# Performance work log

Measured on AMD Instinct MI355X. Metric: run time of the kernel, lower is better.

Reference implementation:

```python
import jax, jax.numpy as jnp
import numpy as np

DIM_Q = 1024
DIM_K = 1024
DIM_V = 1024


def setup_inputs() -> dict:
    key = jax.random.key(0)
    kx, kq, kk, kv = jax.random.split(key, 4)
    x = jax.random.normal(kx, (4, 2048, DIM_Q), dtype=jnp.float32)
    # torch nn.Linear weights: [out_features, in_features], y = x @ W.T
    scale = 1.0 / np.sqrt(DIM_Q)
    Wq = jax.random.uniform(kq, (DIM_K, DIM_Q), dtype=jnp.float32, minval=-scale, maxval=scale)
    Wk = jax.random.uniform(kk, (DIM_K, DIM_Q), dtype=jnp.float32, minval=-scale, maxval=scale)
    Wv = jax.random.uniform(kv, (DIM_V, DIM_Q), dtype=jnp.float32, minval=-scale, maxval=scale)
    return {"x": x, "Wq": Wq, "Wk": Wk, "Wv": Wv}


def reference(x, Wq, Wk, Wv):
    # q, k: [b, s, dim_k]; v: [b, s, dim_v]
    q = jnp.einsum('bsd,kd->bsk', x, Wq)
    k = jnp.einsum('bsd,kd->bsk', x, Wk)
    v = jnp.einsum('bsd,vd->bsv', x, Wv)
    norm_fact = 1.0 / jnp.sqrt(jnp.asarray(DIM_K, dtype=x.dtype))
    score = jnp.einsum('bik,bjk->bij', q, k) * norm_fact  # [b, s, s]
    score = jax.nn.softmax(score, axis=-1)
    att = jnp.einsum('bij,bjv->biv', score, v)
    att = att + v  # is_residual=True
    return att
```

## Files before the change

### kernel.cpp

```cpp
#include <hip/hip_runtime.h>
#include <hip/hip_bf16.h>

using bf16 = __hip_bfloat16;
typedef __attribute__((ext_vector_type(8))) short short8;
typedef __attribute__((ext_vector_type(4))) float floatx4;
typedef __attribute__((ext_vector_type(8))) int int8v;

__device__ __forceinline__ void async_ld16(const void* g, void* l) {
  __builtin_amdgcn_global_load_lds((const __attribute__((address_space(1))) void*)g,
                                   (__attribute__((address_space(3))) void*)l, 16, 0, 0);
}

__device__ __forceinline__ int pk4_fp8(float a, float b, float c, float d) {
  int v = __builtin_amdgcn_cvt_pk_fp8_f32(a, b, 0, false);
  return __builtin_amdgcn_cvt_pk_fp8_f32(c, d, v, true);
}

__device__ __forceinline__ int8v ld_frag16(const unsigned char* lo, const unsigned char* hi) {
  int4 l0 = *(const int4*)lo, h0 = *(const int4*)hi;
  int8v v;
  v[0] = l0.x; v[1] = l0.y; v[2] = l0.z; v[3] = l0.w;
  v[4] = h0.x; v[5] = h0.y; v[6] = h0.z; v[7] = h0.w;
  return v;
}


__device__ __forceinline__ void gemm_core(const bf16* __restrict__ At,
                                          const bf16* __restrict__ Bt,
                                          int K, bf16* lA, bf16* lB,
                                          floatx4 acc[4][4]) {
  const int tid  = threadIdx.x;
  const int w    = tid >> 6;
  const int lane = tid & 63;
  const int subM = (w >> 1) * 64;
  const int subN = (w & 1) * 64;
  const int fr   = lane & 15;
  const int fq   = lane >> 4;

  int srow[4], scol[4], sdst[4];
#pragma unroll
  for (int q = 0; q < 4; ++q) {
    int p = q * 256 + w * 64 + lane;
    int r = p >> 3;
    int j = (p & 7) ^ (r & 7);
    srow[q] = r;
    scol[q] = j * 8;
    sdst[q] = (q * 256 + w * 64) * 8;
  }
  int offA[2][4], offB[2][4];
#pragma unroll
  for (int kc = 0; kc < 2; ++kc)
#pragma unroll
    for (int i = 0; i < 4; ++i) {
      int rA = subM + i * 16 + fr;
      offA[kc][i] = (rA * 8 + ((kc * 4 + fq) ^ (rA & 7))) * 8;
      int rB = subN + i * 16 + fr;
      offB[kc][i] = (rB * 8 + ((kc * 4 + fq) ^ (rB & 7))) * 8;
    }

  floatx4 zero = {0.f, 0.f, 0.f, 0.f};
#pragma unroll
  for (int i = 0; i < 4; ++i)
#pragma unroll
    for (int j = 0; j < 4; ++j) acc[i][j] = zero;

  for (int k0 = 0; k0 < K; k0 += 64) {
    __syncthreads();
#pragma unroll
    for (int q = 0; q < 4; ++q) {
      async_ld16(At + (size_t)srow[q] * K + k0 + scol[q], lA + sdst[q]);
      async_ld16(Bt + (size_t)srow[q] * K + k0 + scol[q], lB + sdst[q]);
    }
    __syncthreads();
#pragma unroll
    for (int kc = 0; kc < 2; ++kc) {
      short8 a[4], b[4];
#pragma unroll
      for (int i = 0; i < 4; ++i) a[i] = *(const short8*)(lA + offA[kc][i]);
#pragma unroll
      for (int j = 0; j < 4; ++j) b[j] = *(const short8*)(lB + offB[kc][j]);
#pragma unroll
      for (int i = 0; i < 4; ++i)
#pragma unroll
        for (int j = 0; j < 4; ++j)
          acc[i][j] = __builtin_amdgcn_mfma_f32_16x16x32_bf16(a[i], b[j], acc[i][j], 0, 0, 0);
    }
  }
}

__device__ __forceinline__ void gemm_core_f8(const unsigned char* __restrict__ At,
                                             const unsigned char* __restrict__ Bt,
                                             int K, unsigned char* lA, unsigned char* lB,
                                             floatx4 acc[4][4]) {
  const int tid  = threadIdx.x;
  const int w    = tid >> 6;
  const int lane = tid & 63;
  const int subM = (w >> 1) * 64;
  const int subN = (w & 1) * 64;
  const int fr   = lane & 15;
  const int fq   = lane >> 4;

  int srow[4], scol[4], sdst[4];
#pragma unroll
  for (int q = 0; q < 4; ++q) {
    int p = q * 256 + w * 64 + lane;
    int r = p >> 3;
    int j = (p & 7) ^ (r & 7) ^ ((r & 8) >> 1);
    srow[q] = r;
    scol[q] = j * 16;
    sdst[q] = (q * 256 + w * 64) * 16;
  }
  int offA[2][4], offB[2][4];
#pragma unroll
  for (int h = 0; h < 2; ++h)
#pragma unroll
    for (int i = 0; i < 4; ++i) {
      int rA = subM + i * 16 + fr;
      offA[h][i] = rA * 128 + (((fq * 2 + h) ^ (rA & 7) ^ ((rA & 8) >> 1)) * 16);
      int rB = subN + i * 16 + fr;
      offB[h][i] = rB * 128 + (((fq * 2 + h) ^ (rB & 7) ^ ((rB & 8) >> 1)) * 16);
    }

  floatx4 zero = {0.f, 0.f, 0.f, 0.f};
#pragma unroll
  for (int i = 0; i < 4; ++i)
#pragma unroll
    for (int j = 0; j < 4; ++j) acc[i][j] = zero;

  for (int k0 = 0; k0 < K; k0 += 128) {
    __syncthreads();
#pragma unroll
    for (int q = 0; q < 4; ++q) {
      async_ld16(At + (size_t)srow[q] * K + k0 + scol[q], lA + sdst[q]);
      async_ld16(Bt + (size_t)srow[q] * K + k0 + scol[q], lB + sdst[q]);
    }
    __syncthreads();
    int8v a[4], b[4];
#pragma unroll
    for (int i = 0; i < 4; ++i) a[i] = ld_frag16(lA + offA[0][i], lA + offA[1][i]);
#pragma unroll
    for (int j = 0; j < 4; ++j) b[j] = ld_frag16(lB + offB[0][j], lB + offB[1][j]);
#pragma unroll
    for (int i = 0; i < 4; ++i)
#pragma unroll
      for (int j = 0; j < 4; ++j)
        acc[i][j] = __builtin_amdgcn_mfma_scale_f32_16x16x128_f8f6f4(
            a[i], b[j], acc[i][j], 0, 0, 0, 0x7F7F7F7F, 0, 0x7F7F7F7F);
  }
}

__device__ __forceinline__ void gemm_core_f8_v2(const unsigned char* __restrict__ At,
                                                const unsigned char* __restrict__ Bt,
                                                int K, unsigned char* lA, unsigned char* lB,
                                                floatx4 acc[4][8]) {
  const int tid  = threadIdx.x;
  const int w    = tid >> 6;
  const int lane = tid & 63;
  const int subM = (w >> 1) * 64;
  const int subN = (w & 1) * 128;
  const int fr   = lane & 15;
  const int fq   = lane >> 4;

  int srowA[4], scolA[4], sdstA[4];
#pragma unroll
  for (int q = 0; q < 4; ++q) {
    int p = q * 256 + w * 64 + lane;
    int r = p >> 3;
    int j = (p & 7) ^ (r & 7) ^ ((r & 8) >> 1);
    srowA[q] = r; scolA[q] = j * 16; sdstA[q] = (q * 256 + w * 64) * 16;
  }
  int srowB[8], scolB[8], sdstB[8];
#pragma unroll
  for (int q = 0; q < 8; ++q) {
    int p = q * 256 + w * 64 + lane;
    int r = p >> 3;
    int j = (p & 7) ^ (r & 7) ^ ((r & 8) >> 1);
    srowB[q] = r; scolB[q] = j * 16; sdstB[q] = (q * 256 + w * 64) * 16;
  }
  int offA[2][4], offB[2][8];
#pragma unroll
  for (int h = 0; h < 2; ++h) {
#pragma unroll
    for (int i = 0; i < 4; ++i) {
      int rA = subM + i * 16 + fr;
      offA[h][i] = rA * 128 + (((fq * 2 + h) ^ (rA & 7) ^ ((rA & 8) >> 1)) * 16);
    }
#pragma unroll
    for (int j = 0; j < 8; ++j) {
      int rB = subN + j * 16 + fr;
      offB[h][j] = rB * 128 + (((fq * 2 + h) ^ (rB & 7) ^ ((rB & 8) >> 1)) * 16);
    }
  }

  floatx4 zero = {0.f, 0.f, 0.f, 0.f};
#pragma unroll
  for (int i = 0; i < 4; ++i)
#pragma unroll
    for (int j = 0; j < 8; ++j) acc[i][j] = zero;

  for (int k0 = 0; k0 < K; k0 += 128) {
    __syncthreads();
#pragma unroll
    for (int q = 0; q < 4; ++q)
      async_ld16(At + (size_t)srowA[q] * K + k0 + scolA[q], lA + sdstA[q]);
#pragma unroll
    for (int q = 0; q < 8; ++q)
      async_ld16(Bt + (size_t)srowB[q] * K + k0 + scolB[q], lB + sdstB[q]);
    __syncthreads();
    int8v a[4];
#pragma unroll
    for (int i = 0; i < 4; ++i) a[i] = ld_frag16(lA + offA[0][i], lA + offA[1][i]);
#pragma unroll
    for (int j = 0; j < 8; ++j) {
      int8v bf = ld_frag16(lB + offB[0][j], lB + offB[1][j]);
#pragma unroll
      for (int i = 0; i < 4; ++i)
        acc[i][j] = __builtin_amdgcn_mfma_scale_f32_16x16x128_f8f6f4(
            a[i], bf, acc[i][j], 0, 0, 0, 0x7F7F7F7F, 0, 0x7F7F7F7F);
    }
  }
}

__global__ __launch_bounds__(256, 2) void proj_gemm(
    const bf16* __restrict__ Xbf, const bf16* __restrict__ Wvbf, bf16* __restrict__ Vbf,
    const unsigned char* __restrict__ X8, const unsigned char* __restrict__ Wq8,
    const unsigned char* __restrict__ Wk8,
    unsigned char* __restrict__ Qf8, unsigned char* __restrict__ Kf8,
    unsigned char* __restrict__ Vt8) {
  __shared__ __align__(16) char lds[49152];
  const int id = blockIdx.x;
  const int tid = threadIdx.x, w = tid >> 6, lane = tid & 63;
  const int fr = lane & 15, fq = lane >> 4;

  if (id < 512) {
    const int r = id & 7, g = id >> 3;
    const int ty = r * 8 + (g & 7), tx = g >> 3;
    bf16* lA = (bf16*)lds;
    bf16* lB = (bf16*)(lds + 16384);
    floatx4 acc[4][4];
    gemm_core(Xbf + (size_t)ty * 128 * 1024, Wvbf + (size_t)tx * 128 * 1024,
              1024, lA, lB, acc);
    const int subM = (w >> 1) * 64, subN = (w & 1) * 64;
    const int rowBase = ty * 128 + subM;
    const int colBase = tx * 128 + subN;
#pragma unroll
    for (int i = 0; i < 4; ++i)
#pragma unroll
      for (int j = 0; j < 4; ++j)
#pragma unroll
        for (int rr = 0; rr < 4; ++rr) {
          int row = rowBase + i * 16 + fq * 4 + rr;
          int col = colBase + j * 16 + fr;
          Vbf[(size_t)row * 1024 + col] = __float2bfloat16(acc[i][j][rr]);
        }

    __syncthreads();
    unsigned int* tp = (unsigned int*)lds;
#pragma unroll
    for (int i = 0; i < 4; ++i) {
      int rw = (subM + i * 16 + fq * 4) >> 2;
#pragma unroll
      for (int j = 0; j < 4; ++j) {
        int c = subN + j * 16 + fr;
        tp[c * 32 + (rw ^ (c & 31))] =
            (unsigned int)pk4_fp8(acc[i][j][0], acc[i][j][1], acc[i][j][2], acc[i][j][3]);
      }
    }
    __syncthreads();
    const int vrow = tid >> 1;
    const int gh = tid & 1;
    size_t ob = ((size_t)((ty >> 4) * 1024 + tx * 128 + vrow)) * 2048 +
                (size_t)(ty & 15) * 128 + gh * 64;
#pragma unroll
    for (int h = 0; h < 4; ++h) {
      unsigned int W0 = tp[vrow * 32 + ((gh * 16 + h) ^ (vrow & 31))];
      unsigned int W1 = tp[vrow * 32 + ((gh * 16 + h + 4) ^ (vrow & 31))];
      unsigned int W2 = tp[vrow * 32 + ((gh * 16 + h + 8) ^ (vrow & 31))];
      unsigned int W3 = tp[vrow * 32 + ((gh * 16 + h + 12) ^ (vrow & 31))];
      unsigned int t01l = __builtin_amdgcn_perm(W1, W0, 0x05010400u);
      unsigned int t01h = __builtin_amdgcn_perm(W1, W0, 0x07030602u);
      unsigned int t23l = __builtin_amdgcn_perm(W3, W2, 0x05010400u);
      unsigned int t23h = __builtin_amdgcn_perm(W3, W2, 0x07030602u);
      uint4 o;
      o.x = __builtin_amdgcn_perm(t23l, t01l, 0x05040100u);
      o.y = __builtin_amdgcn_perm(t23l, t01l, 0x07060302u);
      o.z = __builtin_amdgcn_perm(t23h, t01h, 0x05040100u);
      o.w = __builtin_amdgcn_perm(t23h, t01h, 0x07060302u);
      *(uint4*)&Vt8[ob + h * 16] = o;
    }
  } else {
    const int local = id - 512;
    const int z = local >> 8, lid = local & 255;
    const int r = lid & 7, g = lid >> 3;
    const int ty = r * 8 + (g & 7);
    const int tx = g >> 3;
    unsigned char* lA = (unsigned char*)lds;
    unsigned char* lB = (unsigned char*)(lds + 16384);
    floatx4 acc[4][8];
    gemm_core_f8_v2(X8 + (size_t)ty * 128 * 1024,
                    (z == 0 ? Wq8 : Wk8) + (size_t)tx * 256 * 1024, 1024, lA, lB, acc);
    unsigned char* dst = (z == 0) ? Qf8 : Kf8;
    const int subM = (w >> 1) * 64, subN = (w & 1) * 128;
    const int rowBase = ty * 128 + subM;
    const int colBase = tx * 256 + subN;
#pragma unroll
    for (int i = 0; i < 4; ++i)
#pragma unroll
      for (int rr = 0; rr < 4; ++rr) {
        int row = rowBase + i * 16 + fq * 4 + rr;
        unsigned int p0 = (unsigned int)pk4_fp8(acc[i][0][rr], acc[i][1][rr],
                                                acc[i][2][rr], acc[i][3][rr]);
        unsigned int p1 = (unsigned int)pk4_fp8(acc[i][4][rr], acc[i][5][rr],
                                                acc[i][6][rr], acc[i][7][rr]);
        *(unsigned int*)&dst[(size_t)row * 1024 + colBase + fr * 4] = p0;
        *(unsigned int*)&dst[(size_t)row * 1024 + colBase + 64 + fr * 4] = p1;
      }
  }
}

__global__ __launch_bounds__(256, 2) void mid_kernel(
    const unsigned char* __restrict__ Qf8, const unsigned char* __restrict__ Kf8,
    unsigned char* __restrict__ S8, float* __restrict__ l) {
  __shared__ __align__(16) char lds[49152];
  const int id = blockIdx.x;
  const int t = threadIdx.x;

  const int r = id & 7, g = id >> 3;
  const int b = g >> 4;
  const int rem = g & 15;
  const int ty = r * 2 + (rem & 1);
  const int tx = rem >> 1;
  unsigned char* lA = (unsigned char*)lds;
  unsigned char* lB = (unsigned char*)(lds + 16384);
  floatx4 acc[4][8];
  gemm_core_f8_v2(Qf8 + (size_t)b * 2048 * 1024 + (size_t)ty * 128 * 1024,
                  Kf8 + (size_t)b * 2048 * 1024 + (size_t)tx * 256 * 1024,
                  1024, lA, lB, acc);
  const int w = t >> 6, lane = t & 63;
  const int subM = (w >> 1) * 64, subN = (w & 1) * 128;
  const int fr = lane & 15, fq = lane >> 4;
  const int rowBase = ty * 128 + subM;
  const int colBase = tx * 256 + subN;
  unsigned char* Sb = S8 + (size_t)b * 2048 * 2048;
  float* lb = l + (size_t)b * 2048;
#pragma unroll
  for (int i = 0; i < 4; ++i)
#pragma unroll
    for (int rr = 0; rr < 4; ++rr) {
      int row = rowBase + i * 16 + fq * 4 + rr;
      unsigned int p0 = (unsigned int)pk4_fp8(
          __expf(acc[i][0][rr] * 0.03125f), __expf(acc[i][1][rr] * 0.03125f),
          __expf(acc[i][2][rr] * 0.03125f), __expf(acc[i][3][rr] * 0.03125f));
      unsigned int p1 = (unsigned int)pk4_fp8(
          __expf(acc[i][4][rr] * 0.03125f), __expf(acc[i][5][rr] * 0.03125f),
          __expf(acc[i][6][rr] * 0.03125f), __expf(acc[i][7][rr] * 0.03125f));
      *(unsigned int*)&Sb[(size_t)row * 2048 + colBase + fr * 4] = p0;
      *(unsigned int*)&Sb[(size_t)row * 2048 + colBase + 64 + fr * 4] = p1;
      float psum = __builtin_amdgcn_cvt_f32_fp8(p0, 0) + __builtin_amdgcn_cvt_f32_fp8(p0, 1) +
                   __builtin_amdgcn_cvt_f32_fp8(p0, 2) + __builtin_amdgcn_cvt_f32_fp8(p0, 3) +
                   __builtin_amdgcn_cvt_f32_fp8(p1, 0) + __builtin_amdgcn_cvt_f32_fp8(p1, 1) +
                   __builtin_amdgcn_cvt_f32_fp8(p1, 2) + __builtin_amdgcn_cvt_f32_fp8(p1, 3);
      psum += __shfl_xor(psum, 1, 64);
      psum += __shfl_xor(psum, 2, 64);
      psum += __shfl_xor(psum, 4, 64);
      psum += __shfl_xor(psum, 8, 64);
      if (fr == 0) atomicAdd(&lb[row], psum);
    }
}

__global__ __launch_bounds__(256, 2) void pv_gemm(const unsigned char* __restrict__ S8,
                                                  const unsigned char* __restrict__ Vt8,
                                                  const bf16* __restrict__ Vbf,
                                                  const float* __restrict__ l,
                                                  float* __restrict__ out) {
  __shared__ __align__(16) char lds[32768];
  unsigned char* lA = (unsigned char*)lds;
  unsigned char* lB = (unsigned char*)(lds + 16384);
  const int id = blockIdx.x;
  const int r = id & 7, g = id >> 3;
  const int b = g >> 4;
  const int rem = g & 15;
  const int ty = r * 2 + (rem & 1);
  const int tx = rem >> 1;

  floatx4 acc[4][4];
  gemm_core_f8(S8 + (size_t)b * 2048 * 2048 + (size_t)ty * 128 * 2048,
               Vt8 + (size_t)b * 1024 * 2048 + (size_t)tx * 128 * 2048,
               2048, lA, lB, acc);

  const int tid = threadIdx.x, w = tid >> 6, lane = tid & 63;
  const int subM = (w >> 1) * 64, subN = (w & 1) * 64;
  const int fr = lane & 15, fq = lane >> 4;
  const int rowBase = ty * 128 + subM;
  const int colBase = tx * 128 + subN;
  const float* lb = l + (size_t)b * 2048;
#pragma unroll
  for (int i = 0; i < 4; ++i)
#pragma unroll
    for (int rr = 0; rr < 4; ++rr) {
      int row = rowBase + i * 16 + fq * 4 + rr;
      float inv = 1.0f / lb[row];
#pragma unroll
      for (int j = 0; j < 4; ++j) {
        int col = colBase + j * 16 + fr;
        size_t oi = ((size_t)b * 2048 + row) * 1024 + col;
        out[oi] = acc[i][j][rr] * inv + __bfloat162float(Vbf[oi]);
      }
    }
}

__global__ void cast_all(const float* __restrict__ x, const float* __restrict__ wq,
                         const float* __restrict__ wk, const float* __restrict__ wv,
                         bf16* __restrict__ Xbf, unsigned char* __restrict__ X8,
                         unsigned char* __restrict__ Wq8, unsigned char* __restrict__ Wk8,
                         bf16* __restrict__ Wvbf, float* __restrict__ l) {
  const int blk = blockIdx.x;
  const int t = threadIdx.x;
  if (blk < 2048) {
#pragma unroll
    for (int k = 0; k < 4; ++k) {
      int i = blk * 1024 + k * 256 + t;
      float4 f = ((const float4*)x)[i];
      bf16 tmp[4] = {__float2bfloat16(f.x), __float2bfloat16(f.y),
                     __float2bfloat16(f.z), __float2bfloat16(f.w)};
      ((ushort4*)Xbf)[i] = *(const ushort4*)tmp;
      ((unsigned int*)X8)[i] = (unsigned int)pk4_fp8(f.x, f.y, f.z, f.w);
    }
  } else if (blk < 2560) {
    const float* src = (blk < 2304) ? wq : wk;
    unsigned char* dst = (blk < 2304) ? Wq8 : Wk8;
    int base = ((blk - 2048) & 255) * 1024;
#pragma unroll
    for (int k = 0; k < 4; ++k) {
      int i = base + k * 256 + t;
      float4 f = ((const float4*)src)[i];
      ((unsigned int*)dst)[i] = (unsigned int)pk4_fp8(f.x, f.y, f.z, f.w);
    }
  } else if (blk < 2816) {
#pragma unroll
    for (int k = 0; k < 4; ++k) {
      int i = (blk - 2560) * 1024 + k * 256 + t;
      float4 f = ((const float4*)wv)[i];
      bf16 tmp[4] = {__float2bfloat16(f.x), __float2bfloat16(f.y),
                     __float2bfloat16(f.z), __float2bfloat16(f.w)};
      ((ushort4*)Wvbf)[i] = *(const ushort4*)tmp;
    }
  } else {
#pragma unroll
    for (int k = 0; k < 8; ++k)
      ((float4*)l)[k * 256 + t] = make_float4(0.f, 0.f, 0.f, 0.f);
  }
}

extern "C" void kernel_launch(void* const* d_in, const int* in_sizes, int n_in,
                              void* d_out, int out_size, void* d_ws, size_t ws_size,
                              hipStream_t stream) {
  const float* x  = (const float*)d_in[0];
  const float* Wq = (const float*)d_in[1];
  const float* Wk = (const float*)d_in[2];
  const float* Wv = (const float*)d_in[3];
  float* out = (float*)d_out;

  char* ws = (char*)d_ws;
  bf16* Xbf = (bf16*)ws;                   ws += (size_t)8192 * 1024 * 2;
  unsigned char* X8 = (unsigned char*)ws;  ws += (size_t)8192 * 1024;
  unsigned char* Wq8 = (unsigned char*)ws; ws += (size_t)1024 * 1024;
  unsigned char* Wk8 = (unsigned char*)ws; ws += (size_t)1024 * 1024;
  bf16* Wvbf = (bf16*)ws;                  ws += (size_t)1024 * 1024 * 2;
  unsigned char* Qf8 = (unsigned char*)ws; ws += (size_t)8192 * 1024;
  unsigned char* Kf8 = (unsigned char*)ws; ws += (size_t)8192 * 1024;
  bf16* Vbf = (bf16*)ws;                   ws += (size_t)8192 * 1024 * 2;
  unsigned char* Vt8 = (unsigned char*)ws; ws += (size_t)4 * 1024 * 2048;
  unsigned char* S8  = (unsigned char*)ws; ws += (size_t)4 * 2048 * 2048;
  float* l = (float*)ws;                   ws += (size_t)8192 * 4;

  cast_all<<<2817, 256, 0, stream>>>(x, Wq, Wk, Wv, Xbf, X8, Wq8, Wk8, Wvbf, l);
  proj_gemm<<<1024, 256, 0, stream>>>(Xbf, Wvbf, Vbf, X8, Wq8, Wk8, Qf8, Kf8, Vt8);
  mid_kernel<<<512, 256, 0, stream>>>(Qf8, Kf8, S8, l);
  pv_gemm<<<512, 256, 0, stream>>>(S8, Vt8, Vbf, l, out);
}
```

Before: 179.7 us.

## Use 256x256 double-buffered 8-wave FP8 GEMM core with phased prefetch for QK and scores

Replaces the single-buffered 128x256 FP8 GEMM core with a 256x256, 512-thread variant. It double-buffers LDS (128KB) and splits each K-step into four MFMA phases interleaved with fragment loads and async prefetch of the next tile, using barriers and setprio. The V projection is split out of the fused projection kernel into its own launch, and the Q/K projection and score kernels move to 256 larger blocks. This aims to hide global-load latency and raise data reuse per block, at the cost of one extra launch, lower occupancy from the large LDS, and fewer blocks to fill the CUs.

```diff
diff --git a/kernel.cpp b/kernel.cpp
--- a/kernel.cpp
+++ b/kernel.cpp
@@ -149,217 +149,268 @@
   }
 }
 
-__device__ __forceinline__ void gemm_core_f8_v2(const unsigned char* __restrict__ At,
-                                                const unsigned char* __restrict__ Bt,
-                                                int K, unsigned char* lA, unsigned char* lB,
-                                                floatx4 acc[4][8]) {
+__device__ __forceinline__ void gemm_core_f8_8ph(const unsigned char* __restrict__ At,
+                                                 const unsigned char* __restrict__ Bt,
+                                                 int K, unsigned char* lds0,
+                                                 floatx4 acc[8][4]) {
   const int tid  = threadIdx.x;
   const int w    = tid >> 6;
   const int lane = tid & 63;
-  const int subM = (w >> 1) * 64;
-  const int subN = (w & 1) * 128;
+  const int wr   = w >> 2;
+  const int wc   = w & 3;
+  const int subM = wr * 128;
+  const int subN = wc * 64;
   const int fr   = lane & 15;
   const int fq   = lane >> 4;
 
-  int srowA[4], scolA[4], sdstA[4];
+  int srcOff[4], dstOff[4];
 #pragma unroll
   for (int q = 0; q < 4; ++q) {
-    int p = q * 256 + w * 64 + lane;
+    int p = q * 512 + tid;
     int r = p >> 3;
     int j = (p & 7) ^ (r & 7) ^ ((r & 8) >> 1);
-    srowA[q] = r; scolA[q] = j * 16; sdstA[q] = (q * 256 + w * 64) * 16;
-  }
-  int srowB[8], scolB[8], sdstB[8];
-#pragma unroll
-  for (int q = 0; q < 8; ++q) {
-    int p = q * 256 + w * 64 + lane;
-    int r = p >> 3;
-    int j = (p & 7) ^ (r & 7) ^ ((r & 8) >> 1);
-    srowB[q] = r; scolB[q] = j * 16; sdstB[q] = (q * 256 + w * 64) * 16;
-  }
-  int offA[2][4], offB[2][8];
+    srcOff[q] = r * K + j * 16;
+    dstOff[q] = p * 16;
+  }
+  int offA[2][8], offB[2][4];
 #pragma unroll
   for (int h = 0; h < 2; ++h) {
 #pragma unroll
-    for (int i = 0; i < 4; ++i) {
+    for (int i = 0; i < 8; ++i) {
       int rA = subM + i * 16 + fr;
       offA[h][i] = rA * 128 + (((fq * 2 + h) ^ (rA & 7) ^ ((rA & 8) >> 1)) * 16);
     }
 #pragma unroll
-    for (int j = 0; j < 8; ++j) {
+    for (int j = 0; j < 4; ++j) {
       int rB = subN + j * 16 + fr;
       offB[h][j] = rB * 128 + (((fq * 2 + h) ^ (rB & 7) ^ ((rB & 8) >> 1)) * 16);
     }
   }
 
+  auto stageA = [&](int buf, int k0) {
+#pragma unroll
+    for (int q = 0; q < 4; ++q)
+      async_ld16(At + (size_t)(k0 + srcOff[q]), lds0 + buf * 65536 + dstOff[q]);
+  };
+  auto stageB = [&](int buf, int k0) {
+#pragma unroll
+    for (int q = 0; q < 4; ++q)
+      async_ld16(Bt + (size_t)(k0 + srcOff[q]), lds0 + buf * 65536 + 32768 + dstOff[q]);
+  };
+
   floatx4 zero = {0.f, 0.f, 0.f, 0.f};
 #pragma unroll
-  for (int i = 0; i < 4; ++i)
-#pragma unroll
-    for (int j = 0; j < 8; ++j) acc[i][j] = zero;
-
-  for (int k0 = 0; k0 < K; k0 += 128) {
-    __syncthreads();
-#pragma unroll
-    for (int q = 0; q < 4; ++q)
-      async_ld16(At + (size_t)srowA[q] * K + k0 + scolA[q], lA + sdstA[q]);
-#pragma unroll
-    for (int q = 0; q < 8; ++q)
-      async_ld16(Bt + (size_t)srowB[q] * K + k0 + scolB[q], lB + sdstB[q]);
-    __syncthreads();
-    int8v a[4];
+  for (int i = 0; i < 8; ++i)
+#pragma unroll
+    for (int j = 0; j < 4; ++j) acc[i][j] = zero;
+
+  stageA(0, 0);
+  stageB(0, 0);
+  asm volatile("s_waitcnt vmcnt(0)" ::: "memory");
+  __builtin_amdgcn_s_barrier();
+
+  const int nt = K >> 7;
+  for (int t = 0; t < nt; ++t) {
+    const unsigned char* lA = lds0 + (t & 1) * 65536;
+    const unsigned char* lB = lA + 32768;
+    const int nb = (t + 1) & 1;
+    const int k0n = (t + 1) << 7;
+    const bool pf = (t + 1) < nt;
+    int8v a[4], b0[2], b1[2];
+
 #pragma unroll
     for (int i = 0; i < 4; ++i) a[i] = ld_frag16(lA + offA[0][i], lA + offA[1][i]);
 #pragma unroll
-    for (int j = 0; j < 8; ++j) {
-      int8v bf = ld_frag16(lB + offB[0][j], lB + offB[1][j]);
-#pragma unroll
-      for (int i = 0; i < 4; ++i)
+    for (int j = 0; j < 2; ++j) b0[j] = ld_frag16(lB + offB[0][j], lB + offB[1][j]);
+    if (pf) stageA(nb, k0n);
+    __builtin_amdgcn_s_barrier();
+    asm volatile("s_waitcnt lgkmcnt(0)" ::: "memory");
+    __builtin_amdgcn_sched_barrier(0);
+    __builtin_amdgcn_s_setprio(1);
+#pragma unroll
+    for (int i = 0; i < 4; ++i)
+#pragma unroll
+      for (int j = 0; j < 2; ++j)
         acc[i][j] = __builtin_amdgcn_mfma_scale_f32_16x16x128_f8f6f4(
-            a[i], bf, acc[i][j], 0, 0, 0, 0x7F7F7F7F, 0, 0x7F7F7F7F);
-    }
-  }
-}
-
-__global__ __launch_bounds__(256, 2) void proj_gemm(
+            a[i], b0[j], acc[i][j], 0, 0, 0, 0x7F7F7F7F, 0, 0x7F7F7F7F);
+    __builtin_amdgcn_s_setprio(0);
+    __builtin_amdgcn_s_barrier();
+
+#pragma unroll
+    for (int j = 0; j < 2; ++j) b1[j] = ld_frag16(lB + offB[0][2 + j], lB + offB[1][2 + j]);
+    if (pf) stageB(nb, k0n);
+    __builtin_amdgcn_s_barrier();
+    asm volatile("s_waitcnt lgkmcnt(0)" ::: "memory");
+    __builtin_amdgcn_sched_barrier(0);
+    __builtin_amdgcn_s_setprio(1);
+#pragma unroll
+    for (int i = 0; i < 4; ++i)
+#pragma unroll
+      for (int j = 0; j < 2; ++j)
+        acc[i][2 + j] = __builtin_amdgcn_mfma_scale_f32_16x16x128_f8f6f4(
+            a[i], b1[j], acc[i][2 + j], 0, 0, 0, 0x7F7F7F7F, 0, 0x7F7F7F7F);
+    __builtin_amdgcn_s_setprio(0);
+    __builtin_amdgcn_s_barrier();
+
+#pragma unroll
+    for (int i = 0; i < 4; ++i) a[i] = ld_frag16(lA + offA[0][4 + i], lA + offA[1][4 + i]);
+    __builtin_amdgcn_s_barrier();
+    asm volatile("s_waitcnt lgkmcnt(0)" ::: "memory");
+    __builtin_amdgcn_sched_barrier(0);
+    __builtin_amdgcn_s_setprio(1);
+#pragma unroll
+    for (int i = 0; i < 4; ++i)
+#pragma unroll
+      for (int j = 0; j < 2; ++j)
+        acc[4 + i][2 + j] = __builtin_amdgcn_mfma_scale_f32_16x16x128_f8f6f4(
+            a[i], b1[j], acc[4 + i][2 + j], 0, 0, 0, 0x7F7F7F7F, 0, 0x7F7F7F7F);
+    __builtin_amdgcn_s_setprio(0);
+    __builtin_amdgcn_s_barrier();
+
+#pragma unroll
+    for (int j = 0; j < 2; ++j) b0[j] = ld_frag16(lB + offB[0][j], lB + offB[1][j]);
+    __builtin_amdgcn_s_barrier();
+    asm volatile("s_waitcnt lgkmcnt(0)" ::: "memory");
+    __builtin_amdgcn_sched_barrier(0);
+    __builtin_amdgcn_s_setprio(1);
+#pragma unroll
+    for (int i = 0; i < 4; ++i)
+#pragma unroll
+      for (int j = 0; j < 2; ++j)
+        acc[4 + i][j] = __builtin_amdgcn_mfma_scale_f32_16x16x128_f8f6f4(
+            a[i], b0[j], acc[4 + i][j], 0, 0, 0, 0x7F7F7F7F, 0, 0x7F7F7F7F);
+    __builtin_amdgcn_s_setprio(0);
+    asm volatile("s_waitcnt vmcnt(0)" ::: "memory");
+    __builtin_amdgcn_s_barrier();
+  }
+}
+
+__global__ __launch_bounds__(256, 2) void proj_v(
     const bf16* __restrict__ Xbf, const bf16* __restrict__ Wvbf, bf16* __restrict__ Vbf,
-    const unsigned char* __restrict__ X8, const unsigned char* __restrict__ Wq8,
-    const unsigned char* __restrict__ Wk8,
-    unsigned char* __restrict__ Qf8, unsigned char* __restrict__ Kf8,
     unsigned char* __restrict__ Vt8) {
   __shared__ __align__(16) char lds[49152];
   const int id = blockIdx.x;
   const int tid = threadIdx.x, w = tid >> 6, lane = tid & 63;
   const int fr = lane & 15, fq = lane >> 4;
 
-  if (id < 512) {
-    const int r = id & 7, g = id >> 3;
-    const int ty = r * 8 + (g & 7), tx = g >> 3;
-    bf16* lA = (bf16*)lds;
-    bf16* lB = (bf16*)(lds + 16384);
-    floatx4 acc[4][4];
-    gemm_core(Xbf + (size_t)ty * 128 * 1024, Wvbf + (size_t)tx * 128 * 1024,
-              1024, lA, lB, acc);
-    const int subM = (w >> 1) * 64, subN = (w & 1) * 64;
-    const int rowBase = ty * 128 + subM;
-    const int colBase = tx * 128 + subN;
-#pragma unroll
-    for (int i = 0; i < 4; ++i)
-#pragma unroll
-      for (int j = 0; j < 4; ++j)
-#pragma unroll
-        for (int rr = 0; rr < 4; ++rr) {
-          int row = rowBase + i * 16 + fq * 4 + rr;
-          int col = colBase + j * 16 + fr;
-          Vbf[(size_t)row * 1024 + col] = __float2bfloat16(acc[i][j][rr]);
-        }
-
-    __syncthreads();
-    unsigned int* tp = (unsigned int*)lds;
-#pragma unroll
-    for (int i = 0; i < 4; ++i) {
-      int rw = (subM + i * 16 + fq * 4) >> 2;
-#pragma unroll
-      for (int j = 0; j < 4; ++j) {
-        int c = subN + j * 16 + fr;
-        tp[c * 32 + (rw ^ (c & 31))] =
-            (unsigned int)pk4_fp8(acc[i][j][0], acc[i][j][1], acc[i][j][2], acc[i][j][3]);
-      }
-    }
-    __syncthreads();
-    const int vrow = tid >> 1;
-    const int gh = tid & 1;
-    size_t ob = ((size_t)((ty >> 4) * 1024 + tx * 128 + vrow)) * 2048 +
-                (size_t)(ty & 15) * 128 + gh * 64;
-#pragma unroll
-    for (int h = 0; h < 4; ++h) {
-      unsigned int W0 = tp[vrow * 32 + ((gh * 16 + h) ^ (vrow & 31))];
-      unsigned int W1 = tp[vrow * 32 + ((gh * 16 + h + 4) ^ (vrow & 31))];
-      unsigned int W2 = tp[vrow * 32 + ((gh * 16 + h + 8) ^ (vrow & 31))];
-      unsigned int W3 = tp[vrow * 32 + ((gh * 16 + h + 12) ^ (vrow & 31))];
-      unsigned int t01l = __builtin_amdgcn_perm(W1, W0, 0x05010400u);
-      unsigned int t01h = __builtin_amdgcn_perm(W1, W0, 0x07030602u);
-      unsigned int t23l = __builtin_amdgcn_perm(W3, W2, 0x05010400u);
-      unsigned int t23h = __builtin_amdgcn_perm(W3, W2, 0x07030602u);
-      uint4 o;
-      o.x = __builtin_amdgcn_perm(t23l, t01l, 0x05040100u);
-      o.y = __builtin_amdgcn_perm(t23l, t01l, 0x07060302u);
-      o.z = __builtin_amdgcn_perm(t23h, t01h, 0x05040100u);
-      o.w = __builtin_amdgcn_perm(t23h, t01h, 0x07060302u);
-      *(uint4*)&Vt8[ob + h * 16] = o;
-    }
-  } else {
-    const int local = id - 512;
-    const int z = local >> 8, lid = local & 255;
-    const int r = lid & 7, g = lid >> 3;
-    const int ty = r * 8 + (g & 7);
-    const int tx = g >> 3;
-    unsigned char* lA = (unsigned char*)lds;
-    unsigned char* lB = (unsigned char*)(lds + 16384);
-    floatx4 acc[4][8];
-    gemm_core_f8_v2(X8 + (size_t)ty * 128 * 1024,
-                    (z == 0 ? Wq8 : Wk8) + (size_t)tx * 256 * 1024, 1024, lA, lB, acc);
-    unsigned char* dst = (z == 0) ? Qf8 : Kf8;
-    const int subM = (w >> 1) * 64, subN = (w & 1) * 128;
-    const int rowBase = ty * 128 + subM;
-    const int colBase = tx * 256 + subN;
-#pragma unroll
-    for (int i = 0; i < 4; ++i)
+  const int r = id & 7, g = id >> 3;
+  const int ty = r * 8 + (g & 7), tx = g >> 3;
+  bf16* lA = (bf16*)lds;
+  bf16* lB = (bf16*)(lds + 16384);
+  floatx4 acc[4][4];
+  gemm_core(Xbf + (size_t)ty * 128 * 1024, Wvbf + (size_t)tx * 128 * 1024,
+            1024, lA, lB, acc);
+  const int subM = (w >> 1) * 64, subN = (w & 1) * 64;
+  const int rowBase = ty * 128 + subM;
+  const int colBase = tx * 128 + subN;
+#pragma unroll
+  for (int i = 0; i < 4; ++i)
+#pragma unroll
+    for (int j = 0; j < 4; ++j)
 #pragma unroll
       for (int rr = 0; rr < 4; ++rr) {
         int row = rowBase + i * 16 + fq * 4 + rr;
-        unsigned int p0 = (unsigned int)pk4_fp8(acc[i][0][rr], acc[i][1][rr],
-                                                acc[i][2][rr], acc[i][3][rr]);
-        unsigned int p1 = (unsigned int)pk4_fp8(acc[i][4][rr], acc[i][5][rr],
-                                                acc[i][6][rr], acc[i][7][rr]);
-        *(unsigned int*)&dst[(size_t)row * 1024 + colBase + fr * 4] = p0;
-        *(unsigned int*)&dst[(size_t)row * 1024 + colBase + 64 + fr * 4] = p1;
+        int col = colBase + j * 16 + fr;
+        Vbf[(size_t)row * 1024 + col] = __float2bfloat16(acc[i][j][rr]);
       }
-  }
-}
-
-__global__ __launch_bounds__(256, 2) void mid_kernel(
+
+  __syncthreads();
+  unsigned int* tp = (unsigned int*)lds;
+#pragma unroll
+  for (int i = 0; i < 4; ++i) {
+    int rw = (subM + i * 16 + fq * 4) >> 2;
+#pragma unroll
+    for (int j = 0; j < 4; ++j) {
+      int c = subN + j * 16 + fr;
+      tp[c * 32 + (rw ^ (c & 31))] =
+          (unsigned int)pk4_fp8(acc[i][j][0], acc[i][j][1], acc[i][j][2], acc[i][j][3]);
+    }
+  }
+  __syncthreads();
+  const int vrow = tid >> 1;
+  const int gh = tid & 1;
+  size_t ob = ((size_t)((ty >> 4) * 1024 + tx * 128 + vrow)) * 2048 +
+              (size_t)(ty & 15) * 128 + gh * 64;
+#pragma unroll
+  for (int h = 0; h < 4; ++h) {
+    unsigned int W0 = tp[vrow * 32 + ((gh * 16 + h) ^ (vrow & 31))];
+    unsigned int W1 = tp[vrow * 32 + ((gh * 16 + h + 4) ^ (vrow & 31))];
+    unsigned int W2 = tp[vrow * 32 + ((gh * 16 + h + 8) ^ (vrow & 31))];
+    unsigned int W3 = tp[vrow * 32 + ((gh * 16 + h + 12) ^ (vrow & 31))];
+    unsigned int t01l = __builtin_amdgcn_perm(W1, W0, 0x05010400u);
+    unsigned int t01h = __builtin_amdgcn_perm(W1, W0, 0x07030602u);
+    unsigned int t23l = __builtin_amdgcn_perm(W3, W2, 0x05010400u);
+    unsigned int t23h = __builtin_amdgcn_perm(W3, W2, 0x07030602u);
+    uint4 o;
+    o.x = __builtin_amdgcn_perm(t23l, t01l, 0x05040100u);
+    o.y = __builtin_amdgcn_perm(t23l, t01l, 0x07060302u);
+    o.z = __builtin_amdgcn_perm(t23h, t01h, 0x05040100u);
+    o.w = __builtin_amdgcn_perm(t23h, t01h, 0x07060302u);
+    *(uint4*)&Vt8[ob + h * 16] = o;
+  }
+}
+
+__global__ __launch_bounds__(512, 2) void proj_qk(
+    const unsigned char* __restrict__ X8, const unsigned char* __restrict__ Wq8,
+    const unsigned char* __restrict__ Wk8,
+    unsigned char* __restrict__ Qf8, unsigned char* __restrict__ Kf8) {
+  __shared__ __align__(16) char lds[131072];
+  const int id = blockIdx.x;
+  const int z = id >> 7, lid = id & 127;
+  const int ty = lid >> 2, tx = lid & 3;
+
+  floatx4 acc[8][4];
+  gemm_core_f8_8ph(X8 + (size_t)ty * 256 * 1024,
+                   (z == 0 ? Wq8 : Wk8) + (size_t)tx * 256 * 1024,
+                   1024, (unsigned char*)lds, acc);
+
+  unsigned char* dst = (z == 0) ? Qf8 : Kf8;
+  const int tid = threadIdx.x, w = tid >> 6, lane = tid & 63;
+  const int wr = w >> 2, wc = w & 3;
+  const int fr = lane & 15, fq = lane >> 4;
+  const int rowBase = ty * 256 + wr * 128;
+  const int colBase = tx * 256 + wc * 64;
+#pragma unroll
+  for (int i = 0; i < 8; ++i)
+#pragma unroll
+    for (int rr = 0; rr < 4; ++rr) {
+      int row = rowBase + i * 16 + fq * 4 + rr;
+      unsigned int p0 = (unsigned int)pk4_fp8(acc[i][0][rr], acc[i][1][rr],
+                                              acc[i][2][rr], acc[i][3][rr]);
+      *(unsigned int*)&dst[(size_t)row * 1024 + colBase + fr * 4] = p0;
+    }
+}
+
+__global__ __launch_bounds__(512, 2) void mid_kernel(
     const unsigned char* __restrict__ Qf8, const unsigned char* __restrict__ Kf8,
     unsigned char* __restrict__ S8, float* __restrict__ l) {
-  __shared__ __align__(16) char lds[49152];
+  __shared__ __align__(16) char lds[131072];
   const int id = blockIdx.x;
-  const int t = threadIdx.x;
-
-  const int r = id & 7, g = id >> 3;
-  const int b = g >> 4;
-  const int rem = g & 15;
-  const int ty = r * 2 + (rem & 1);
-  const int tx = rem >> 1;
-  unsigned char* lA = (unsigned char*)lds;
-  unsigned char* lB = (unsigned char*)(lds + 16384);
-  floatx4 acc[4][8];
-  gemm_core_f8_v2(Qf8 + (size_t)b * 2048 * 1024 + (size_t)ty * 128 * 1024,
-                  Kf8 + (size_t)b * 2048 * 1024 + (size_t)tx * 256 * 1024,
-                  1024, lA, lB, acc);
-  const int w = t >> 6, lane = t & 63;
-  const int subM = (w >> 1) * 64, subN = (w & 1) * 128;
+  const int b = id >> 6, ty = (id >> 3) & 7, tx = id & 7;
+
+  floatx4 acc[8][4];
+  gemm_core_f8_8ph(Qf8 + (size_t)b * 2048 * 1024 + (size_t)ty * 256 * 1024,
+                   Kf8 + (size_t)b * 2048 * 1024 + (size_t)tx * 256 * 1024,
+                   1024, (unsigned char*)lds, acc);
+
+  const int tid = threadIdx.x, w = tid >> 6, lane = tid & 63;
+  const int wr = w >> 2, wc = w & 3;
   const int fr = lane & 15, fq = lane >> 4;
-  const int rowBase = ty * 128 + subM;
-  const int colBase = tx * 256 + subN;
+  const int rowBase = ty * 256 + wr * 128;
+  const int colBase = tx * 256 + wc * 64;
   unsigned char* Sb = S8 + (size_t)b * 2048 * 2048;
   float* lb = l + (size_t)b * 2048;
 #pragma unroll
-  for (int i = 0; i < 4; ++i)
+  for (int i = 0; i < 8; ++i)
 #pragma unroll
     for (int rr = 0; rr < 4; ++rr) {
       int row = rowBase + i * 16 + fq * 4 + rr;
       unsigned int p0 = (unsigned int)pk4_fp8(
           __expf(acc[i][0][rr] * 0.03125f), __expf(acc[i][1][rr] * 0.03125f),
           __expf(acc[i][2][rr] * 0.03125f), __expf(acc[i][3][rr] * 0.03125f));
-      unsigned int p1 = (unsigned int)pk4_fp8(
-          __expf(acc[i][4][rr] * 0.03125f), __expf(acc[i][5][rr] * 0.03125f),
-          __expf(acc[i][6][rr] * 0.03125f), __expf(acc[i][7][rr] * 0.03125f));
       *(unsigned int*)&Sb[(size_t)row * 2048 + colBase + fr * 4] = p0;
-      *(unsigned int*)&Sb[(size_t)row * 2048 + colBase + 64 + fr * 4] = p1;
       float psum = __builtin_amdgcn_cvt_f32_fp8(p0, 0) + __builtin_amdgcn_cvt_f32_fp8(p0, 1) +
-                   __builtin_amdgcn_cvt_f32_fp8(p0, 2) + __builtin_amdgcn_cvt_f32_fp8(p0, 3) +
-                   __builtin_amdgcn_cvt_f32_fp8(p1, 0) + __builtin_amdgcn_cvt_f32_fp8(p1, 1) +
-                   __builtin_amdgcn_cvt_f32_fp8(p1, 2) + __builtin_amdgcn_cvt_f32_fp8(p1, 3);
+                   __builtin_amdgcn_cvt_f32_fp8(p0, 2) + __builtin_amdgcn_cvt_f32_fp8(p0, 3);
       psum += __shfl_xor(psum, 1, 64);
       psum += __shfl_xor(psum, 2, 64);
       psum += __shfl_xor(psum, 4, 64);
@@ -475,7 +526,8 @@
   float* l = (float*)ws;                   ws += (size_t)8192 * 4;
 
   cast_all<<<2817, 256, 0, stream>>>(x, Wq, Wk, Wv, Xbf, X8, Wq8, Wk8, Wvbf, l);
-  proj_gemm<<<1024, 256, 0, stream>>>(Xbf, Wvbf, Vbf, X8, Wq8, Wk8, Qf8, Kf8, Vt8);
-  mid_kernel<<<512, 256, 0, stream>>>(Qf8, Kf8, S8, l);
+  proj_v<<<512, 256, 0, stream>>>(Xbf, Wvbf, Vbf, Vt8);
+  proj_qk<<<256, 512, 0, stream>>>(X8, Wq8, Wk8, Qf8, Kf8);
+  mid_kernel<<<256, 512, 0, stream>>>(Qf8, Kf8, S8, l);
   pv_gemm<<<512, 256, 0, stream>>>(S8, Vt8, Vbf, l, out);
 }
```

Result: slower. 188.1 us (+4.7%).
